# Kernel tuning notes

Measured on AMD Instinct MI355X. Metric: run time of the kernel, lower is better.

The kernel has to match this reference:

```python
import jax, jax.numpy as jnp
import numpy as np

B, T, E = 2, 2048, 768
H = 12
HD = E // H          # 64
ROT = 32             # rotary dim (= head_dim // 2 in CLVP)
SCALE = HD ** -0.5


def rotate_half(x):
    # split last dim into (2, d/2), rotate second half by 90 deg
    x = x.reshape(*x.shape[:-1], 2, x.shape[-1] // 2)
    x1, x2 = x[..., 0, :], x[..., 1, :]
    return jnp.concatenate([-x2, x1], axis=-1)


def apply_rotary_pos_emb(state, freqs):
    # state: (B*H, T, HD); freqs: (1, T, ROT)
    pos_emb_len = freqs.shape[-1]
    s_l, s_r = state[..., :pos_emb_len], state[..., pos_emb_len:]
    f = freqs[:, :, -s_l.shape[-1]:]
    s_l = s_l * jnp.cos(f) + rotate_half(s_l) * jnp.sin(f)
    return jnp.concatenate([s_l, s_r], axis=-1)


def setup_inputs() -> dict:
    key = jax.random.key(0)
    ks = jax.random.split(key, 6)
    hidden_states = jax.random.normal(ks[0], (B, T, E), dtype=jnp.float32)
    rotary_pos_emb = jax.random.uniform(ks[1], (1, T, ROT), dtype=jnp.float32)
    Wq = jax.random.normal(ks[2], (E, E), dtype=jnp.float32) * 0.02
    Wk = jax.random.normal(ks[3], (E, E), dtype=jnp.float32) * 0.02
    Wv = jax.random.normal(ks[4], (E, E), dtype=jnp.float32) * 0.02
    Wo = jax.random.normal(ks[5], (E, E), dtype=jnp.float32) * 0.02
    bo = jnp.zeros((E,), dtype=jnp.float32)
    return {"hidden_states": hidden_states, "rotary_pos_emb": rotary_pos_emb,
            "Wq": Wq, "Wk": Wk, "Wv": Wv, "Wo": Wo, "bo": bo}


def _shape(x):
    # (B, T, E) -> (B*H, T, HD)
    return x.reshape(B, T, H, HD).transpose(0, 2, 1, 3).reshape(B * H, T, HD)


def reference(hidden_states, rotary_pos_emb, Wq, Wk, Wv, Wo, bo):
    # nn.Linear: x @ W.T
    q = _shape(hidden_states @ Wq.T * SCALE)
    k = _shape(hidden_states @ Wk.T)
    v = _shape(hidden_states @ Wv.T)

    q = apply_rotary_pos_emb(q, rotary_pos_emb)
    k = apply_rotary_pos_emb(k, rotary_pos_emb)
    v = apply_rotary_pos_emb(v, rotary_pos_emb)  # CLVP applies RoPE to V too

    attn = jax.nn.softmax(jnp.einsum('bqd,bkd->bqk', q, k), axis=-1)  # (B*H, T, T)
    out = jnp.einsum('bqk,bkd->bqd', attn, v)                          # (B*H, T, HD)
    out = out.reshape(B, H, T, HD).transpose(0, 2, 1, 3).reshape(B, T, E)
    return out @ Wo.T + bo
```

## Files before the change

kernel.cpp:

```cpp
#include <hip/hip_runtime.h>
#include <hip/hip_bf16.h>

typedef unsigned short ushort_t;
typedef __attribute__((ext_vector_type(8))) short short8;
typedef __attribute__((ext_vector_type(4))) float f32x4;

constexpr int B  = 2;
constexpr int T  = 2048;
constexpr int E  = 768;
constexpr int H  = 12;
constexpr int HD = 64;
constexpr float QSCALE = 0.125f * 1.44269504088896f;

__device__ __forceinline__ ushort_t f2bf(float x) {
  unsigned int u = __float_as_uint(x);
  u += 0x7fffu + ((u >> 16) & 1u);
  return (ushort_t)(u >> 16);
}

__device__ __forceinline__ unsigned int pack_bf2(float a, float b) {
  __hip_bfloat162 h = __float22bfloat162_rn(float2{a, b});
  return *(unsigned int*)&h;
}

__device__ __forceinline__ int swz(int row, int col) {
  return row * 64 + ((((col >> 3) ^ (row & 7)) << 3) | (col & 7));
}

__device__ __forceinline__ void gl_lds16(const ushort_t* g, ushort_t* l) {
  __builtin_amdgcn_global_load_lds(
      (const __attribute__((address_space(1))) unsigned int*)g,
      (__attribute__((address_space(3))) unsigned int*)l, 16, 0, 0);
}

__global__ __launch_bounds__(256) void cvt_all(
    const float* __restrict__ X,  const float* __restrict__ Wq,
    const float* __restrict__ Wk, const float* __restrict__ Wv,
    const float* __restrict__ Wo, const float* __restrict__ rope,
    ushort_t* __restrict__ Xb,  ushort_t* __restrict__ Wqb,
    ushort_t* __restrict__ Wkb, ushort_t* __restrict__ Wvb,
    ushort_t* __restrict__ Wob, float* __restrict__ ct, float* __restrict__ st)
{
  constexpr int NX4 = (B * T * E) / 4;
  constexpr int NW4 = (E * E) / 4;
  constexpr int NC4 = NX4 + 4 * NW4;
  int i = blockIdx.x * 256 + threadIdx.x;
  if (i < NC4) {
    const float* s; ushort_t* d; int j;
    if (i < NX4) { s = X; d = Xb; j = i; }
    else {
      int t = i - NX4;
      int w = t / NW4; j = t - w * NW4;
      s = (w == 0) ? Wq : (w == 1) ? Wk : (w == 2) ? Wv : Wo;
      d = (w == 0) ? Wqb : (w == 1) ? Wkb : (w == 2) ? Wvb : Wob;
    }
    float4 v = ((const float4*)s)[j];
    ushort4 o;
    o.x = f2bf(v.x); o.y = f2bf(v.y); o.z = f2bf(v.z); o.w = f2bf(v.w);
    ((ushort4*)d)[j] = o;
  } else {
    int j = (i - NC4) * 4;
    float4 f = *(const float4*)(rope + j);
    float c, s;
    sincosf(f.x, &s, &c); ct[j+0] = c; st[j+0] = s;
    sincosf(f.y, &s, &c); ct[j+1] = c; st[j+1] = s;
    sincosf(f.z, &s, &c); ct[j+2] = c; st[j+2] = s;
    sincosf(f.w, &s, &c); ct[j+3] = c; st[j+3] = s;
  }
}

__global__ __launch_bounds__(256) void qkv_gemm(
    const ushort_t* __restrict__ Xb,
    const ushort_t* __restrict__ Wqb, const ushort_t* __restrict__ Wkb,
    const ushort_t* __restrict__ Wvb,
    const float* __restrict__ ct, const float* __restrict__ st,
    ushort_t* __restrict__ qfb, ushort_t* __restrict__ kfb, ushort_t* __restrict__ vfb)
{
  __shared__ __align__(16) ushort_t smem[128 * 64 + 64 * 64];
  ushort_t* Xs = smem;
  ushort_t* Ws = smem + 128 * 64;
  const int tid  = threadIdx.x;
  const int wave = tid >> 6;
  const int lane = tid & 63;
  const int l15  = lane & 15, quad = lane >> 4;
  const int n0 = blockIdx.x * 64;
  const int m0 = blockIdx.y * 128;
  const int z  = blockIdx.z;
  const ushort_t* Wt = (z == 0) ? Wqb : (z == 1) ? Wkb : Wvb;
  const int h = n0 >> 6;

  f32x4 acc[2][4];
  #pragma unroll
  for (int i = 0; i < 2; ++i)
    #pragma unroll
    for (int j = 0; j < 4; ++j) acc[i][j] = (f32x4){0.f, 0.f, 0.f, 0.f};

  const int li8 = lane >> 3, lc8 = lane & 7;
  const ushort_t* gX[4]; ushort_t* lX[4];
  #pragma unroll
  for (int j = 0; j < 4; ++j) {
    int row = wave * 32 + j * 8 + li8;
    int c = lc8 ^ (row & 7);
    gX[j] = Xb + (size_t)(m0 + row) * E + c * 8;
    lX[j] = Xs + (wave * 32 + j * 8) * 64;
  }
  const ushort_t* gW[2]; ushort_t* lW[2];
  #pragma unroll
  for (int j = 0; j < 2; ++j) {
    int row = wave * 16 + j * 8 + li8;
    int c = lc8 ^ (row & 7);
    gW[j] = Wt + (size_t)(n0 + row) * E + c * 8;
    lW[j] = Ws + (wave * 16 + j * 8) * 64;
  }

  for (int k0 = 0; k0 < E; k0 += 64) {
    #pragma unroll
    for (int j = 0; j < 4; ++j) gl_lds16(gX[j] + k0, lX[j]);
    #pragma unroll
    for (int j = 0; j < 2; ++j) gl_lds16(gW[j] + k0, lW[j]);
    __syncthreads();
    short8 a[2][2];
    #pragma unroll
    for (int mt = 0; mt < 2; ++mt)
      #pragma unroll
      for (int kh = 0; kh < 2; ++kh)
        a[mt][kh] = *(const short8*)&Xs[swz(wave * 32 + mt * 16 + l15, kh * 32 + quad * 8)];
    #pragma unroll
    for (int nt = 0; nt < 4; ++nt) {
      #pragma unroll
      for (int kh = 0; kh < 2; ++kh) {
        short8 bb = *(const short8*)&Ws[swz(nt * 16 + l15, kh * 32 + quad * 8)];
        #pragma unroll
        for (int mt = 0; mt < 2; ++mt)
          acc[mt][nt] = __builtin_amdgcn_mfma_f32_16x16x32_bf16(a[mt][kh], bb, acc[mt][nt], 0, 0, 0);
      }
    }
    __syncthreads();
  }

  const int b  = m0 >> 11;
  const int t0 = m0 & (T - 1);
  const int bh = b * H + h;
  const float qscale = (z == 0) ? QSCALE : 1.0f;

  if (z < 2) {
    #pragma unroll
    for (int mt = 0; mt < 2; ++mt) {
      #pragma unroll
      for (int r = 0; r < 4; ++r) {
        int mloc = wave * 32 + mt * 16 + quad * 4 + r;
        int t = (m0 + mloc) & (T - 1);
        float s0 = acc[mt][0][r] * qscale;
        float s1 = acc[mt][1][r] * qscale;
        float c0v = ct[t * 32 + l15],      sn0 = st[t * 32 + l15];
        float c1v = ct[t * 32 + 16 + l15], sn1 = st[t * 32 + 16 + l15];
        smem[swz(mloc, l15)]      = f2bf(s0 * c0v - s1 * sn0);
        smem[swz(mloc, 16 + l15)] = f2bf(s1 * c1v + s0 * sn1);
        smem[swz(mloc, 32 + l15)] = f2bf(acc[mt][2][r] * qscale);
        smem[swz(mloc, 48 + l15)] = f2bf(acc[mt][3][r] * qscale);
      }
    }
    __syncthreads();
    if (z == 0) {
      #pragma unroll
      for (int i = 0; i < 4; ++i) {
        int p = tid + 256 * i;
        int qtl = p >> 7, kh = (p >> 6) & 1, ln = p & 63;
        int tl = qtl * 16 + (ln & 15);
        int d  = kh * 32 + (ln >> 4) * 8;
        uint4 v = *(const uint4*)&smem[swz(tl, d)];
        size_t off = ((size_t)((bh * 128 + (t0 >> 4) + qtl) * 2 + kh)) * 512 + ln * 8;
        *(uint4*)(qfb + off) = v;
      }
    } else {
      #pragma unroll
      for (int i = 0; i < 4; ++i) {
        int p = tid + 256 * i;
        int ktl = p >> 9, mt = (p >> 7) & 3, kh = (p >> 6) & 1, ln = p & 63;
        int tl = ktl * 64 + mt * 16 + (ln & 15);
        int d  = kh * 32 + (ln >> 4) * 8;
        uint4 v = *(const uint4*)&smem[swz(tl, d)];
        size_t off = ((size_t)(((bh * 32 + (t0 >> 6) + ktl) * 4 + mt) * 2 + kh)) * 512 + ln * 8;
        *(uint4*)(kfb + off) = v;
      }
    }
  } else {
    #pragma unroll
    for (int mt = 0; mt < 2; ++mt) {
      #pragma unroll
      for (int r = 0; r < 4; ++r) {
        int mloc = wave * 32 + mt * 16 + quad * 4 + r;
        int t = (m0 + mloc) & (T - 1);
        float s0 = acc[mt][0][r], s1 = acc[mt][1][r];
        float c0v = ct[t * 32 + l15],      sn0 = st[t * 32 + l15];
        float c1v = ct[t * 32 + 16 + l15], sn1 = st[t * 32 + 16 + l15];
        smem[(l15)      * 132 + mloc] = f2bf(s0 * c0v - s1 * sn0);
        smem[(16 + l15) * 132 + mloc] = f2bf(s1 * c1v + s0 * sn1);
        smem[(32 + l15) * 132 + mloc] = f2bf(acc[mt][2][r]);
        smem[(48 + l15) * 132 + mloc] = f2bf(acc[mt][3][r]);
      }
    }
    __syncthreads();
    #pragma unroll
    for (int i = 0; i < 4; ++i) {
      int p = tid + 256 * i;
      int ktl = p >> 9, nt = (p >> 7) & 3, kh = (p >> 6) & 1, ln = p & 63;
      int d  = nt * 16 + (ln & 15);
      int tl = ktl * 64 + kh * 32 + (ln >> 4) * 8;
      uint4 v = *(const uint4*)&smem[d * 132 + tl];
      size_t off = ((size_t)(((bh * 32 + (t0 >> 6) + ktl) * 4 + nt) * 2 + kh)) * 512 + ln * 8;
      *(uint4*)(vfb + off) = v;
    }
  }
}

__global__ __launch_bounds__(256) void attn_kernel(
    const ushort_t* __restrict__ qfb, const ushort_t* __restrict__ kfb,
    const ushort_t* __restrict__ vfb, ushort_t* __restrict__ cbuf)
{
  __shared__ __align__(16) ushort_t Ps[4][32 * 40];
  __shared__ __align__(16) float Osh[2][32][66];
  __shared__ float Lsh[2][32];
  const int tid  = threadIdx.x;
  const int wave = tid >> 6;
  const int wq = wave >> 1, wk = wave & 1;
  const int lane = tid & 63;
  const int l15  = lane & 15, quad = lane >> 4;
  const int q0 = blockIdx.x * 64;
  const int bh = blockIdx.y;
  const ushort_t* Qf = qfb + (size_t)bh * (T * HD);
  const ushort_t* Kf = kfb + (size_t)bh * (T * HD);
  const ushort_t* Vf = vfb + (size_t)bh * (T * HD);
  ushort_t* Pw = &Ps[wave][0];

  short8 qa[2][2];
  #pragma unroll
  for (int qg = 0; qg < 2; ++qg)
    #pragma unroll
    for (int kh = 0; kh < 2; ++kh)
      qa[qg][kh] = *(const short8*)(Qf + ((size_t)(((q0 >> 4) + wq * 2 + qg) * 2 + kh)) * 512 + lane * 8);

  short8 ka[2][2], va[4];
  #pragma unroll
  for (int i = 0; i < 2; ++i)
    #pragma unroll
    for (int kh = 0; kh < 2; ++kh)
      ka[i][kh] = *(const short8*)(Kf + ((size_t)((wk * 2 + i) * 2 + kh)) * 512 + lane * 8);
  #pragma unroll
  for (int nt = 0; nt < 4; ++nt)
    va[nt] = *(const short8*)(Vf + ((size_t)(nt * 2 + wk)) * 512 + lane * 8);

  f32x4 o[2][4];
  #pragma unroll
  for (int qg = 0; qg < 2; ++qg)
    #pragma unroll
    for (int nt = 0; nt < 4; ++nt) o[qg][nt] = (f32x4){0.f, 0.f, 0.f, 0.f};
  float lsum[2] = {0.f, 0.f};

  for (int kt = 0; kt < T / 64; ++kt) {
    const int ktn = (kt + 1 < T / 64) ? kt + 1 : kt;
    short8 kn[2][2], vn[4];
    #pragma unroll
    for (int i = 0; i < 2; ++i)
      #pragma unroll
      for (int kh = 0; kh < 2; ++kh)
        kn[i][kh] = *(const short8*)(Kf + ((size_t)((ktn * 4 + wk * 2 + i) * 2 + kh)) * 512 + lane * 8);
    #pragma unroll
    for (int nt = 0; nt < 4; ++nt)
      vn[nt] = *(const short8*)(Vf + ((size_t)((ktn * 4 + nt) * 2 + wk)) * 512 + lane * 8);

    f32x4 ss[2][2];
    #pragma unroll
    for (int mt = 0; mt < 2; ++mt)
      #pragma unroll
      for (int qg = 0; qg < 2; ++qg) {
        ss[mt][qg] = (f32x4){0.f, 0.f, 0.f, 0.f};
        ss[mt][qg] = __builtin_amdgcn_mfma_f32_16x16x32_bf16(ka[mt][0], qa[qg][0], ss[mt][qg], 0, 0, 0);
        ss[mt][qg] = __builtin_amdgcn_mfma_f32_16x16x32_bf16(ka[mt][1], qa[qg][1], ss[mt][qg], 0, 0, 0);
      }

    #pragma unroll
    for (int qg = 0; qg < 2; ++qg) {
      #pragma unroll
      for (int mt = 0; mt < 2; ++mt) {
        float p0 = exp2f(ss[mt][qg][0]);
        float p1 = exp2f(ss[mt][qg][1]);
        float p2 = exp2f(ss[mt][qg][2]);
        float p3 = exp2f(ss[mt][qg][3]);
        lsum[qg] += (p0 + p1) + (p2 + p3);
        uint2 w2;
        w2.x = pack_bf2(p0, p1);
        w2.y = pack_bf2(p2, p3);
        *(uint2*)&Pw[(qg * 16 + l15) * 40 + mt * 16 + quad * 4] = w2;
      }
    }

    short8 pa0 = *(const short8*)&Pw[(l15) * 40 + quad * 8];
    short8 pa1 = *(const short8*)&Pw[(16 + l15) * 40 + quad * 8];
    #pragma unroll
    for (int nt = 0; nt < 4; ++nt) {
      o[0][nt] = __builtin_amdgcn_mfma_f32_16x16x32_bf16(pa0, va[nt], o[0][nt], 0, 0, 0);
      o[1][nt] = __builtin_amdgcn_mfma_f32_16x16x32_bf16(pa1, va[nt], o[1][nt], 0, 0, 0);
    }

    #pragma unroll
    for (int i = 0; i < 2; ++i) {
      ka[i][0] = kn[i][0];
      ka[i][1] = kn[i][1];
    }
    #pragma unroll
    for (int nt = 0; nt < 4; ++nt) va[nt] = vn[nt];
  }

  #pragma unroll
  for (int qg = 0; qg < 2; ++qg) {
    lsum[qg] += __shfl_xor(lsum[qg], 16);
    lsum[qg] += __shfl_xor(lsum[qg], 32);
  }

  if (wk == 0) {
    #pragma unroll
    for (int qg = 0; qg < 2; ++qg)
      #pragma unroll
      for (int nt = 0; nt < 4; ++nt)
        #pragma unroll
        for (int r = 0; r < 4; ++r)
          Osh[wq][qg * 16 + quad * 4 + r][nt * 16 + l15] = o[qg][nt][r];
    if (lane < 16) {
      Lsh[wq][l15]      = lsum[0];
      Lsh[wq][16 + l15] = lsum[1];
    }
  }
  __syncthreads();
  if (wk == 1) {
    const int b = bh / H, h = bh % H;
    #pragma unroll
    for (int qg = 0; qg < 2; ++qg) {
      float ltot = lsum[qg] + Lsh[wq][qg * 16 + l15];
      float inv0 = 1.0f / ltot;
      #pragma unroll
      for (int r = 0; r < 4; ++r) {
        float inv = __shfl(inv0, quad * 4 + r);
        int t = q0 + wq * 32 + qg * 16 + quad * 4 + r;
        size_t base = ((size_t)b * T + t) * E + h * HD;
        #pragma unroll
        for (int nt = 0; nt < 4; ++nt) {
          float v = o[qg][nt][r] + Osh[wq][qg * 16 + quad * 4 + r][nt * 16 + l15];
          cbuf[base + nt * 16 + l15] = f2bf(v * inv);
        }
      }
    }
  }
}

__global__ __launch_bounds__(256) void out_gemm(
    const ushort_t* __restrict__ Xc, const ushort_t* __restrict__ Wob,
    const float* __restrict__ bo, float* __restrict__ out)
{
  __shared__ __align__(16) ushort_t Xs[128 * 64];
  __shared__ __align__(16) ushort_t Ws[64 * 64];
  const int tid  = threadIdx.x;
  const int wave = tid >> 6;
  const int lane = tid & 63;
  const int l15  = lane & 15, quad = lane >> 4;
  const int n0 = blockIdx.x * 64;
  const int m0 = blockIdx.y * 128;

  f32x4 acc[2][4];
  #pragma unroll
  for (int i = 0; i < 2; ++i)
    #pragma unroll
    for (int j = 0; j < 4; ++j) acc[i][j] = (f32x4){0.f, 0.f, 0.f, 0.f};

  const int li8 = lane >> 3, lc8 = lane & 7;
  const ushort_t* gX[4]; ushort_t* lX[4];
  #pragma unroll
  for (int j = 0; j < 4; ++j) {
    int row = wave * 32 + j * 8 + li8;
    int c = lc8 ^ (row & 7);
    gX[j] = Xc + (size_t)(m0 + row) * E + c * 8;
    lX[j] = Xs + (wave * 32 + j * 8) * 64;
  }
  const ushort_t* gW[2]; ushort_t* lW[2];
  #pragma unroll
  for (int j = 0; j < 2; ++j) {
    int row = wave * 16 + j * 8 + li8;
    int c = lc8 ^ (row & 7);
    gW[j] = Wob + (size_t)(n0 + row) * E + c * 8;
    lW[j] = Ws + (wave * 16 + j * 8) * 64;
  }

  for (int k0 = 0; k0 < E; k0 += 64) {
    #pragma unroll
    for (int j = 0; j < 4; ++j) gl_lds16(gX[j] + k0, lX[j]);
    #pragma unroll
    for (int j = 0; j < 2; ++j) gl_lds16(gW[j] + k0, lW[j]);
    __syncthreads();
    short8 a[2][2];
    #pragma unroll
    for (int mt = 0; mt < 2; ++mt)
      #pragma unroll
      for (int kh = 0; kh < 2; ++kh)
        a[mt][kh] = *(const short8*)&Xs[swz(wave * 32 + mt * 16 + l15, kh * 32 + quad * 8)];
    #pragma unroll
    for (int nt = 0; nt < 4; ++nt) {
      #pragma unroll
      for (int kh = 0; kh < 2; ++kh) {
        short8 bb = *(const short8*)&Ws[swz(nt * 16 + l15, kh * 32 + quad * 8)];
        #pragma unroll
        for (int mt = 0; mt < 2; ++mt)
          acc[mt][nt] = __builtin_amdgcn_mfma_f32_16x16x32_bf16(a[mt][kh], bb, acc[mt][nt], 0, 0, 0);
      }
    }
    __syncthreads();
  }

  float bias[4];
  #pragma unroll
  for (int nt = 0; nt < 4; ++nt) bias[nt] = bo[n0 + nt * 16 + l15];
  #pragma unroll
  for (int mt = 0; mt < 2; ++mt) {
    #pragma unroll
    for (int r = 0; r < 4; ++r) {
      int m = m0 + wave * 32 + mt * 16 + quad * 4 + r;
      float* op = out + (size_t)m * E + n0;
      op[l15]      = acc[mt][0][r] + bias[0];
      op[16 + l15] = acc[mt][1][r] + bias[1];
      op[32 + l15] = acc[mt][2][r] + bias[2];
      op[48 + l15] = acc[mt][3][r] + bias[3];
    }
  }
}

extern "C" void kernel_launch(void* const* d_in, const int* in_sizes, int n_in,
                              void* d_out, int out_size, void* d_ws, size_t ws_size,
                              hipStream_t stream) {
  (void)in_sizes; (void)n_in; (void)out_size; (void)ws_size;
  const float* X    = (const float*)d_in[0];
  const float* rope = (const float*)d_in[1];
  const float* Wq   = (const float*)d_in[2];
  const float* Wk   = (const float*)d_in[3];
  const float* Wv   = (const float*)d_in[4];
  const float* Wo   = (const float*)d_in[5];
  const float* bo   = (const float*)d_in[6];
  float* out = (float*)d_out;

  const size_t NX = (size_t)B * T * E;
  const size_t NW = (size_t)E * E;
  const size_t NR = (size_t)T * 32;
  ushort_t* Xb  = (ushort_t*)d_ws;
  ushort_t* Wqb = Xb  + NX;
  ushort_t* Wkb = Wqb + NW;
  ushort_t* Wvb = Wkb + NW;
  ushort_t* Wob = Wvb + NW;
  ushort_t* qfb = Wob + NW;
  ushort_t* kfb = qfb + NX;
  ushort_t* vfb = kfb + NX;
  ushort_t* cb  = vfb + NX;
  float* ct = (float*)(cb + NX);
  float* st = ct + NR;

  const int total4 = (int)((NX + 4 * NW + NR) / 4);
  cvt_all<<<total4 / 256, 256, 0, stream>>>(X, Wq, Wk, Wv, Wo, rope,
                                            Xb, Wqb, Wkb, Wvb, Wob, ct, st);

  qkv_gemm<<<dim3(E / 64, (B * T) / 128, 3), 256, 0, stream>>>(
      Xb, Wqb, Wkb, Wvb, ct, st, qfb, kfb, vfb);
  attn_kernel<<<dim3(T / 64, B * H), 256, 0, stream>>>(qfb, kfb, vfb, cb);
  out_gemm<<<dim3(E / 64, (B * T) / 128), 256, 0, stream>>>(cb, Wob, bo, out);
}
```

Baseline: 168.8 us.

## Fuse Q/K/V projections into one block per head to reuse X tile

The QKV GEMM now computes all three projections in each block, loading the X tile once and three weight tiles per k-step instead of launching a separate z-slice per projection. This cuts redundant X loads and the block count by a factor of three, but raises the accumulator register count to 96 floats and the LDS use, which may lower occupancy. Separately, the log2(e) factor is dropped from the Q scale and the attention softmax switches from exp2f to __expf, which is mathematically equivalent but likely compiles to an extra multiply per exponent.

```diff
diff --git a/kernel.cpp b/kernel.cpp
--- a/kernel.cpp
+++ b/kernel.cpp
@@ -10,7 +10,7 @@
 constexpr int E  = 768;
 constexpr int H  = 12;
 constexpr int HD = 64;
-constexpr float QSCALE = 0.125f * 1.44269504088896f;
+constexpr float QSCALE = 0.125f;
 
 __device__ __forceinline__ ushort_t f2bf(float x) {
   unsigned int u = __float_as_uint(x);
@@ -76,24 +76,25 @@
     const float* __restrict__ ct, const float* __restrict__ st,
     ushort_t* __restrict__ qfb, ushort_t* __restrict__ kfb, ushort_t* __restrict__ vfb)
 {
-  __shared__ __align__(16) ushort_t smem[128 * 64 + 64 * 64];
+  __shared__ __align__(16) ushort_t smem[128 * 64 + 3 * 64 * 64];
   ushort_t* Xs = smem;
-  ushort_t* Ws = smem + 128 * 64;
+  ushort_t* Ws[3] = { smem + 8192, smem + 8192 + 4096, smem + 8192 + 8192 };
   const int tid  = threadIdx.x;
   const int wave = tid >> 6;
   const int lane = tid & 63;
   const int l15  = lane & 15, quad = lane >> 4;
-  const int n0 = blockIdx.x * 64;
+  const int h  = blockIdx.x;
+  const int n0 = h * 64;
   const int m0 = blockIdx.y * 128;
-  const int z  = blockIdx.z;
-  const ushort_t* Wt = (z == 0) ? Wqb : (z == 1) ? Wkb : Wvb;
-  const int h = n0 >> 6;
-
-  f32x4 acc[2][4];
-  #pragma unroll
-  for (int i = 0; i < 2; ++i)
-    #pragma unroll
-    for (int j = 0; j < 4; ++j) acc[i][j] = (f32x4){0.f, 0.f, 0.f, 0.f};
+  const ushort_t* Wsrc[3] = { Wqb, Wkb, Wvb };
+
+  f32x4 acc[3][2][4];
+  #pragma unroll
+  for (int z = 0; z < 3; ++z)
+    #pragma unroll
+    for (int i = 0; i < 2; ++i)
+      #pragma unroll
+      for (int j = 0; j < 4; ++j) acc[z][i][j] = (f32x4){0.f, 0.f, 0.f, 0.f};
 
   const int li8 = lane >> 3, lc8 = lane & 7;
   const ushort_t* gX[4]; ushort_t* lX[4];
@@ -104,20 +105,24 @@
     gX[j] = Xb + (size_t)(m0 + row) * E + c * 8;
     lX[j] = Xs + (wave * 32 + j * 8) * 64;
   }
-  const ushort_t* gW[2]; ushort_t* lW[2];
-  #pragma unroll
-  for (int j = 0; j < 2; ++j) {
-    int row = wave * 16 + j * 8 + li8;
-    int c = lc8 ^ (row & 7);
-    gW[j] = Wt + (size_t)(n0 + row) * E + c * 8;
-    lW[j] = Ws + (wave * 16 + j * 8) * 64;
-  }
+  const ushort_t* gW[3][2]; ushort_t* lW[3][2];
+  #pragma unroll
+  for (int z = 0; z < 3; ++z)
+    #pragma unroll
+    for (int j = 0; j < 2; ++j) {
+      int row = wave * 16 + j * 8 + li8;
+      int c = lc8 ^ (row & 7);
+      gW[z][j] = Wsrc[z] + (size_t)(n0 + row) * E + c * 8;
+      lW[z][j] = Ws[z] + (wave * 16 + j * 8) * 64;
+    }
 
   for (int k0 = 0; k0 < E; k0 += 64) {
     #pragma unroll
     for (int j = 0; j < 4; ++j) gl_lds16(gX[j] + k0, lX[j]);
     #pragma unroll
-    for (int j = 0; j < 2; ++j) gl_lds16(gW[j] + k0, lW[j]);
+    for (int z = 0; z < 3; ++z)
+      #pragma unroll
+      for (int j = 0; j < 2; ++j) gl_lds16(gW[z][j] + k0, lW[z][j]);
     __syncthreads();
     short8 a[2][2];
     #pragma unroll
@@ -126,38 +131,40 @@
       for (int kh = 0; kh < 2; ++kh)
         a[mt][kh] = *(const short8*)&Xs[swz(wave * 32 + mt * 16 + l15, kh * 32 + quad * 8)];
     #pragma unroll
-    for (int nt = 0; nt < 4; ++nt) {
-      #pragma unroll
-      for (int kh = 0; kh < 2; ++kh) {
-        short8 bb = *(const short8*)&Ws[swz(nt * 16 + l15, kh * 32 + quad * 8)];
+    for (int z = 0; z < 3; ++z)
+      #pragma unroll
+      for (int nt = 0; nt < 4; ++nt)
         #pragma unroll
-        for (int mt = 0; mt < 2; ++mt)
-          acc[mt][nt] = __builtin_amdgcn_mfma_f32_16x16x32_bf16(a[mt][kh], bb, acc[mt][nt], 0, 0, 0);
-      }
-    }
+        for (int kh = 0; kh < 2; ++kh) {
+          short8 bb = *(const short8*)&Ws[z][swz(nt * 16 + l15, kh * 32 + quad * 8)];
+          #pragma unroll
+          for (int mt = 0; mt < 2; ++mt)
+            acc[z][mt][nt] = __builtin_amdgcn_mfma_f32_16x16x32_bf16(a[mt][kh], bb, acc[z][mt][nt], 0, 0, 0);
+        }
     __syncthreads();
   }
 
   const int b  = m0 >> 11;
   const int t0 = m0 & (T - 1);
   const int bh = b * H + h;
-  const float qscale = (z == 0) ? QSCALE : 1.0f;
-
-  if (z < 2) {
+
+  #pragma unroll
+  for (int z = 0; z < 2; ++z) {
+    const float sc = (z == 0) ? QSCALE : 1.0f;
     #pragma unroll
     for (int mt = 0; mt < 2; ++mt) {
       #pragma unroll
       for (int r = 0; r < 4; ++r) {
         int mloc = wave * 32 + mt * 16 + quad * 4 + r;
         int t = (m0 + mloc) & (T - 1);
-        float s0 = acc[mt][0][r] * qscale;
-        float s1 = acc[mt][1][r] * qscale;
+        float s0 = acc[z][mt][0][r] * sc;
+        float s1 = acc[z][mt][1][r] * sc;
         float c0v = ct[t * 32 + l15],      sn0 = st[t * 32 + l15];
         float c1v = ct[t * 32 + 16 + l15], sn1 = st[t * 32 + 16 + l15];
         smem[swz(mloc, l15)]      = f2bf(s0 * c0v - s1 * sn0);
         smem[swz(mloc, 16 + l15)] = f2bf(s1 * c1v + s0 * sn1);
-        smem[swz(mloc, 32 + l15)] = f2bf(acc[mt][2][r] * qscale);
-        smem[swz(mloc, 48 + l15)] = f2bf(acc[mt][3][r] * qscale);
+        smem[swz(mloc, 32 + l15)] = f2bf(acc[z][mt][2][r] * sc);
+        smem[swz(mloc, 48 + l15)] = f2bf(acc[z][mt][3][r] * sc);
       }
     }
     __syncthreads();
@@ -184,33 +191,34 @@
         *(uint4*)(kfb + off) = v;
       }
     }
-  } else {
-    #pragma unroll
-    for (int mt = 0; mt < 2; ++mt) {
-      #pragma unroll
-      for (int r = 0; r < 4; ++r) {
-        int mloc = wave * 32 + mt * 16 + quad * 4 + r;
-        int t = (m0 + mloc) & (T - 1);
-        float s0 = acc[mt][0][r], s1 = acc[mt][1][r];
-        float c0v = ct[t * 32 + l15],      sn0 = st[t * 32 + l15];
-        float c1v = ct[t * 32 + 16 + l15], sn1 = st[t * 32 + 16 + l15];
-        smem[(l15)      * 132 + mloc] = f2bf(s0 * c0v - s1 * sn0);
-        smem[(16 + l15) * 132 + mloc] = f2bf(s1 * c1v + s0 * sn1);
-        smem[(32 + l15) * 132 + mloc] = f2bf(acc[mt][2][r]);
-        smem[(48 + l15) * 132 + mloc] = f2bf(acc[mt][3][r]);
-      }
-    }
-    __syncthreads();
-    #pragma unroll
-    for (int i = 0; i < 4; ++i) {
-      int p = tid + 256 * i;
-      int ktl = p >> 9, nt = (p >> 7) & 3, kh = (p >> 6) & 1, ln = p & 63;
-      int d  = nt * 16 + (ln & 15);
-      int tl = ktl * 64 + kh * 32 + (ln >> 4) * 8;
-      uint4 v = *(const uint4*)&smem[d * 132 + tl];
-      size_t off = ((size_t)(((bh * 32 + (t0 >> 6) + ktl) * 4 + nt) * 2 + kh)) * 512 + ln * 8;
-      *(uint4*)(vfb + off) = v;
-    }
+    __syncthreads();
+  }
+
+  #pragma unroll
+  for (int mt = 0; mt < 2; ++mt) {
+    #pragma unroll
+    for (int r = 0; r < 4; ++r) {
+      int mloc = wave * 32 + mt * 16 + quad * 4 + r;
+      int t = (m0 + mloc) & (T - 1);
+      float s0 = acc[2][mt][0][r], s1 = acc[2][mt][1][r];
+      float c0v = ct[t * 32 + l15],      sn0 = st[t * 32 + l15];
+      float c1v = ct[t * 32 + 16 + l15], sn1 = st[t * 32 + 16 + l15];
+      smem[(l15)      * 132 + mloc] = f2bf(s0 * c0v - s1 * sn0);
+      smem[(16 + l15) * 132 + mloc] = f2bf(s1 * c1v + s0 * sn1);
+      smem[(32 + l15) * 132 + mloc] = f2bf(acc[2][mt][2][r]);
+      smem[(48 + l15) * 132 + mloc] = f2bf(acc[2][mt][3][r]);
+    }
+  }
+  __syncthreads();
+  #pragma unroll
+  for (int i = 0; i < 4; ++i) {
+    int p = tid + 256 * i;
+    int ktl = p >> 9, nt = (p >> 7) & 3, kh = (p >> 6) & 1, ln = p & 63;
+    int d  = nt * 16 + (ln & 15);
+    int tl = ktl * 64 + kh * 32 + (ln >> 4) * 8;
+    uint4 v = *(const uint4*)&smem[d * 132 + tl];
+    size_t off = ((size_t)(((bh * 32 + (t0 >> 6) + ktl) * 4 + nt) * 2 + kh)) * 512 + ln * 8;
+    *(uint4*)(vfb + off) = v;
   }
 }
 
@@ -283,10 +291,10 @@
     for (int qg = 0; qg < 2; ++qg) {
       #pragma unroll
       for (int mt = 0; mt < 2; ++mt) {
-        float p0 = exp2f(ss[mt][qg][0]);
-        float p1 = exp2f(ss[mt][qg][1]);
-        float p2 = exp2f(ss[mt][qg][2]);
-        float p3 = exp2f(ss[mt][qg][3]);
+        float p0 = __expf(ss[mt][qg][0]);
+        float p1 = __expf(ss[mt][qg][1]);
+        float p2 = __expf(ss[mt][qg][2]);
+        float p3 = __expf(ss[mt][qg][3]);
         lsum[qg] += (p0 + p1) + (p2 + p3);
         uint2 w2;
         w2.x = pack_bf2(p0, p1);
@@ -464,7 +472,7 @@
   cvt_all<<<total4 / 256, 256, 0, stream>>>(X, Wq, Wk, Wv, Wo, rope,
                                             Xb, Wqb, Wkb, Wvb, Wob, ct, st);
 
-  qkv_gemm<<<dim3(E / 64, (B * T) / 128, 3), 256, 0, stream>>>(
+  qkv_gemm<<<dim3(H, (B * T) / 128), 256, 0, stream>>>(
       Xb, Wqb, Wkb, Wvb, ct, st, qfb, kfb, vfb);
   attn_kernel<<<dim3(T / 64, B * H), 256, 0, stream>>>(qfb, kfb, vfb, cb);
   out_gemm<<<dim3(E / 64, (B * T) / 128), 256, 0, stream>>>(cb, Wob, bo, out);
```

Result: faster. 162.6 us (-3.7%).
